# Optimization experiments

Hardware: AMD Instinct MI355X
Metric: run time of the kernel (lower is better)

Reference implementation:

```python
import jax, jax.numpy as jnp
import numpy as np

H = 8          # n_heads
D_HEAD = 64    # head_dim; scores scaled by sqrt(D_HEAD)


def setup_inputs() -> dict:
    key = jax.random.key(0)
    ks = jax.random.split(key, 9)
    B, S, Dm = 8, 1024, 512
    return {
        "input_Q": jax.random.normal(ks[0], (B, S, Dm), jnp.float32),
        "input_K": jax.random.normal(ks[1], (B, S, Dm), jnp.float32),
        "input_V": jax.random.normal(ks[2], (B, S, Dm), jnp.float32),
        "attn_mask": jax.random.randint(ks[3], (B, S, S), 0, 2).astype(bool),
        "edge_encoding": jax.random.normal(ks[4], (B, S, S), jnp.float32),
        "W_Q": jax.random.normal(ks[5], (Dm, Dm), jnp.float32) / np.sqrt(Dm),
        "W_K": jax.random.normal(ks[6], (Dm, Dm), jnp.float32) / np.sqrt(Dm),
        "W_V": jax.random.normal(ks[7], (Dm, Dm), jnp.float32) / np.sqrt(Dm),
        "W_fc": jax.random.normal(ks[8], (Dm, Dm), jnp.float32) / np.sqrt(Dm),
    }


def reference(input_Q, input_K, input_V, attn_mask, edge_encoding, W_Q, W_K, W_V, W_fc):
    B, S, Dm = input_Q.shape
    # project and split heads: [B, H, S, d_head]
    def heads(x, W):
        return (x @ W).reshape(B, S, H, D_HEAD).transpose(0, 2, 1, 3)
    Q = heads(input_Q, W_Q)
    K = heads(input_K, W_K)
    V = heads(input_V, W_V)
    scores = jnp.einsum("bhqd,bhkd->bhqk", Q, K) / np.sqrt(D_HEAD)
    scores = scores + edge_encoding[:, None, :, :]
    scores = jnp.where(attn_mask[:, None, :, :], jnp.float32(-1e9), scores)
    attn = jax.nn.softmax(scores, axis=-1)
    context = jnp.einsum("bhqk,bhkd->bhqd", attn, V)
    context = context.transpose(0, 2, 1, 3).reshape(B, S, Dm)
    output = context @ W_fc
    scores_avg = scores.sum(axis=1) / H  # [B, S, S]
    return output, scores_avg
```

## Files before the change

kernel.cpp:

```cpp
#include <hip/hip_runtime.h>
#include <math.h>

#define B_ 8
#define S_ 1024
#define DM 512
#define H_ 8
#define DH 64

typedef _Float16 h4 __attribute__((ext_vector_type(4)));
typedef _Float16 h8 __attribute__((ext_vector_type(8)));
typedef float f4 __attribute__((ext_vector_type(4)));

#define MFMA16(a, b, c) __builtin_amdgcn_mfma_f32_16x16x32_f16(a, b, c, 0, 0, 0)

__global__ __launch_bounds__(256) void cast_x(
    const float* __restrict__ x0, const float* __restrict__ x1,
    const float* __restrict__ x2, _Float16* __restrict__ y0,
    _Float16* __restrict__ y1, _Float16* __restrict__ y2) {
  const float* x = (blockIdx.y == 0) ? x0 : (blockIdx.y == 1) ? x1 : x2;
  _Float16* y = (blockIdx.y == 0) ? y0 : (blockIdx.y == 1) ? y1 : y2;
  size_t i = (size_t)blockIdx.x * 1024 + (size_t)threadIdx.x * 4;
  float4 v = *(const float4*)(x + i);
  h4 hv = {(_Float16)v.x, (_Float16)v.y, (_Float16)v.z, (_Float16)v.w};
  *(h4*)(y + i) = hv;
}

__global__ __launch_bounds__(256) void cast_w(
    const float* __restrict__ w0, const float* __restrict__ w1,
    const float* __restrict__ w2, const float* __restrict__ w3,
    _Float16* __restrict__ t0, _Float16* __restrict__ t1,
    _Float16* __restrict__ t2, _Float16* __restrict__ t3) {
  const float* W;
  _Float16* T;
  switch (blockIdx.z) {
    case 0: W = w0; T = t0; break;
    case 1: W = w1; T = t1; break;
    case 2: W = w2; T = t2; break;
    default: W = w3; T = t3; break;
  }
  __shared__ _Float16 ts[64][72];
  const int t = threadIdx.x;
  const int r = t >> 2, c0 = (t & 3) * 16;
  const int n0 = blockIdx.x * 64, k0 = blockIdx.y * 64;
#pragma unroll
  for (int i = 0; i < 4; i++) {
    float4 v = *(const float4*)&W[(size_t)(k0 + r) * 512 + n0 + c0 + i * 4];
    h4 hv = {(_Float16)v.x, (_Float16)v.y, (_Float16)v.z, (_Float16)v.w};
    *(h4*)&ts[r][c0 + i * 4] = hv;
  }
  __syncthreads();
  alignas(16) _Float16 outv[16];
#pragma unroll
  for (int i = 0; i < 16; i++) outv[i] = ts[c0 + i][r];
  *(uint4*)&T[(size_t)(n0 + r) * 512 + k0 + c0] = *(uint4*)&outv[0];
  *(uint4*)&T[(size_t)(n0 + r) * 512 + k0 + c0 + 8] = *(uint4*)&outv[8];
}

__global__ __launch_bounds__(256) void gemm_qkv(
    const _Float16* __restrict__ Xq, const _Float16* __restrict__ Xk,
    const _Float16* __restrict__ Xv, const _Float16* __restrict__ Wt,
    _Float16* __restrict__ Qh, _Float16* __restrict__ Kh,
    _Float16* __restrict__ Vth) {
  const int z = blockIdx.z;
  const int id = blockIdx.x + 4 * blockIdx.y;
  const int c = id & 7, r = id >> 3;
  const int by = c + 8 * (r & 7);
  const int bx = r >> 3;
  const _Float16* A = (z == 0) ? Xq : (z == 1) ? Xk : Xv;
  const _Float16* Bt = Wt + (size_t)z * 512 * 512;
  __shared__ _Float16 Sh[128 * 144];
  const int t = threadIdx.x, lane = t & 63, w = t >> 6;
  const int quad = lane >> 4, l16 = lane & 15;
  const int row0 = by * 128, col0 = bx * 128;
  const int wm = (w & 1) * 64, wn = (w >> 1) * 64;
  f4 acc[4][4] = {};
  const _Float16* Ab = A + (size_t)(row0 + wm + l16) * DM + quad * 8;
  const _Float16* Bb = Bt + (size_t)(col0 + wn + l16) * DM + quad * 8;
  for (int k0 = 0; k0 < DM; k0 += 64) {
    h8 af[4][2], bf[4][2];
#pragma unroll
    for (int m = 0; m < 4; m++) {
      const _Float16* ap = Ab + (size_t)m * 16 * DM + k0;
      const _Float16* bp = Bb + (size_t)m * 16 * DM + k0;
      af[m][0] = *(const h8*)ap;
      af[m][1] = *(const h8*)(ap + 32);
      bf[m][0] = *(const h8*)bp;
      bf[m][1] = *(const h8*)(bp + 32);
    }
#pragma unroll
    for (int m = 0; m < 4; m++)
#pragma unroll
      for (int n = 0; n < 4; n++) {
        acc[m][n] = MFMA16(af[m][0], bf[n][0], acc[m][n]);
        acc[m][n] = MFMA16(af[m][1], bf[n][1], acc[m][n]);
      }
  }
  if (z < 2) {
    _Float16* C = (z == 0) ? Qh : Kh;
#pragma unroll
    for (int m = 0; m < 4; m++)
#pragma unroll
      for (int n = 0; n < 4; n++)
#pragma unroll
        for (int reg = 0; reg < 4; reg++)
          Sh[(wm + m * 16 + quad * 4 + reg) * 144 + wn + n * 16 + l16] =
              (_Float16)acc[m][n][reg];
    __syncthreads();
    const int rr = t >> 4;
    const int cs = (t & 15) * 8;
#pragma unroll
    for (int i = 0; i < 8; i++) {
      int row = rr + 16 * i;
      *(uint4*)&C[(size_t)(row0 + row) * DM + col0 + cs] =
          *(uint4*)&Sh[row * 144 + cs];
    }
  } else {
#pragma unroll
    for (int m = 0; m < 4; m++)
#pragma unroll
      for (int n = 0; n < 4; n++) {
        h4 vv = {(_Float16)acc[m][n][0], (_Float16)acc[m][n][1],
                 (_Float16)acc[m][n][2], (_Float16)acc[m][n][3]};
        *(h4*)&Sh[(wn + n * 16 + l16) * 144 + wm + m * 16 + quad * 4] = vv;
      }
    __syncthreads();
    const int rr = t >> 4;
    const int cs = (t & 15) * 8;
    const int b = row0 >> 10, s0 = row0 & 1023;
#pragma unroll
    for (int i = 0; i < 8; i++) {
      int cg = col0 + rr + 16 * i;
      int h = cg >> 6, d = cg & 63;
      *(uint4*)&Vth[((size_t)(b * 8 + h) * 64 + d) * S_ + s0 + cs] =
          *(uint4*)&Sh[(rr + 16 * i) * 144 + cs];
    }
  }
}

__global__ __launch_bounds__(256) void gemm_fc(
    const _Float16* __restrict__ A, const _Float16* __restrict__ Bt,
    float* __restrict__ C) {
  const int id = blockIdx.x + 4 * blockIdx.y;
  const int c = id & 7, r = id >> 3;
  const int by = c + 8 * (r & 15);
  const int bx = r >> 4;
  const int t = threadIdx.x, lane = t & 63, w = t >> 6;
  const int quad = lane >> 4, l16 = lane & 15;
  const int row0 = by * 64, col0 = bx * 128;
  const int wm = (w & 1) * 32, wn = (w >> 1) * 64;
  f4 acc[2][4] = {};
  const _Float16* Ab = A + (size_t)(row0 + wm + l16) * DM + quad * 8;
  const _Float16* Bb = Bt + (size_t)(col0 + wn + l16) * DM + quad * 8;
  for (int k0 = 0; k0 < DM; k0 += 64) {
    h8 af[2][2], bf[4][2];
#pragma unroll
    for (int m = 0; m < 2; m++) {
      const _Float16* ap = Ab + (size_t)m * 16 * DM + k0;
      af[m][0] = *(const h8*)ap;
      af[m][1] = *(const h8*)(ap + 32);
    }
#pragma unroll
    for (int n = 0; n < 4; n++) {
      const _Float16* bp = Bb + (size_t)n * 16 * DM + k0;
      bf[n][0] = *(const h8*)bp;
      bf[n][1] = *(const h8*)(bp + 32);
    }
#pragma unroll
    for (int m = 0; m < 2; m++)
#pragma unroll
      for (int n = 0; n < 4; n++) {
        acc[m][n] = MFMA16(af[m][0], bf[n][0], acc[m][n]);
        acc[m][n] = MFMA16(af[m][1], bf[n][1], acc[m][n]);
      }
  }
#pragma unroll
  for (int m = 0; m < 2; m++)
#pragma unroll
    for (int n = 0; n < 4; n++)
#pragma unroll
      for (int reg = 0; reg < 4; reg++) {
        size_t row = row0 + wm + m * 16 + quad * 4 + reg;
        size_t col = col0 + wn + n * 16 + l16;
        C[row * DM + col] = acc[m][n][reg];
      }
}

__global__ __launch_bounds__(256) void scores_mfma(
    const _Float16* __restrict__ Qh, const _Float16* __restrict__ Kh,
    const int* __restrict__ mask, const float* __restrict__ edge,
    float* __restrict__ out1, _Float16* __restrict__ Ehs) {
  const int b = blockIdx.z;
  const int id = blockIdx.x + 8 * blockIdx.y;
  const int iy = id & 7, jx = id >> 3;
  const int i0 = iy * 128, j0 = jx * 128;
  const _Float16* A = Qh + (size_t)b * S_ * DM;
  const _Float16* Bt = Kh + (size_t)b * S_ * DM;
  const int t = threadIdx.x, lane = t & 63, w = t >> 6;
  const int quad = lane >> 4, l16 = lane & 15;
  const int wm = (w & 1) * 64, wn = (w >> 1) * 64;
  f4 acc[4][4] = {};
  const _Float16* Ab = A + (size_t)(i0 + wm + l16) * DM + quad * 8;
  const _Float16* Bb = Bt + (size_t)(j0 + wn + l16) * DM + quad * 8;
  for (int k0 = 0; k0 < DM; k0 += 64) {
    h8 af[4][2], bf[4][2];
#pragma unroll
    for (int m = 0; m < 4; m++) {
      const _Float16* ap = Ab + (size_t)m * 16 * DM + k0;
      const _Float16* bp = Bb + (size_t)m * 16 * DM + k0;
      af[m][0] = *(const h8*)ap;
      af[m][1] = *(const h8*)(ap + 32);
      bf[m][0] = *(const h8*)bp;
      bf[m][1] = *(const h8*)(bp + 32);
    }
#pragma unroll
    for (int m = 0; m < 4; m++)
#pragma unroll
      for (int n = 0; n < 4; n++) {
        acc[m][n] = MFMA16(af[m][0], bf[n][0], acc[m][n]);
        acc[m][n] = MFMA16(af[m][1], bf[n][1], acc[m][n]);
      }
  }
  const int jt_base = j0 >> 6;
#pragma unroll
  for (int m = 0; m < 4; m++)
#pragma unroll
    for (int reg = 0; reg < 4; reg++) {
      size_t gi = i0 + wm + m * 16 + quad * 4 + reg;
      size_t rowb = ((size_t)b * S_ + gi) * S_;
      const int jt = jt_base + (wn >> 6);
      size_t ehrow = (((size_t)b * 16 + jt) * 1024 + gi) * 64 + l16 * 4;
      h4 ev;
#pragma unroll
      for (int n = 0; n < 4; n++) {
        size_t idx = rowb + j0 + wn + n * 16 + l16;
        int mk = mask[idx];
        float e = edge[idx];
        out1[idx] = mk ? -1e9f : (acc[m][n][reg] * (1.0f / 64.0f) + e);
        ev[n] = mk ? (_Float16)(-65504.0f) : (_Float16)e;
      }
      *(h4*)&Ehs[ehrow] = ev;
    }
}

__global__ __launch_bounds__(256) void flash_mfma(
    const _Float16* __restrict__ Qh, const _Float16* __restrict__ Kh,
    const _Float16* __restrict__ Vth, const _Float16* __restrict__ Ehs,
    _Float16* __restrict__ ctxh) {
  __shared__ _Float16 Ps[128][72], Ks[64][72], Vt[64][72];
  const int t = threadIdx.x, lane = t & 63, w = t >> 6;
  const int quad = lane >> 4, l16 = lane & 15;
  const int g = blockIdx.x + 8 * blockIdx.y;
  const int c = g & 7, r = g >> 3;
  const int bh = c + 8 * (r & 7);
  const int qb = r >> 3;
  const int b = bh >> 3, h = bh & 7;
  const int q0 = qb * 128;
  const size_t bS = (size_t)b * S_;
  const int sr = t >> 3, sc = (t & 7) * 8;
  const int qw = w * 32;

#pragma unroll
  for (int i = 0; i < 4; i++)
    *(uint4*)&Ps[sr + 32 * i][sc] =
        *(const uint4*)&Qh[(bS + q0 + sr + 32 * i) * DM + h * DH + sc];
  __syncthreads();
  h8 aq[2][2];
#pragma unroll
  for (int m = 0; m < 2; m++)
#pragma unroll
    for (int k = 0; k < 2; k++)
      aq[m][k] = *(h8*)&Ps[qw + m * 16 + l16][k * 32 + quad * 8];

  uint4 kv[4];
  kv[0] = *(const uint4*)&Kh[(bS + sr) * DM + h * DH + sc];
  kv[1] = *(const uint4*)&Kh[(bS + sr + 32) * DM + h * DH + sc];
  kv[2] = *(const uint4*)&Vth[((size_t)bh * 64 + sr) * S_ + sc];
  kv[3] = *(const uint4*)&Vth[((size_t)bh * 64 + sr + 32) * S_ + sc];
  h4 evh[2][4];
#pragma unroll
  for (int m = 0; m < 2; m++)
#pragma unroll
    for (int reg = 0; reg < 4; reg++)
      evh[m][reg] = *(const h4*)&Ehs[(((size_t)b * 16 + 0) * 1024 + q0 + qw +
                                      m * 16 + quad * 4 + reg) *
                                         64 +
                                     l16 * 4];

  f4 acco[2][4] = {};
  float m_run[2][4], l_run[2][4];
#pragma unroll
  for (int m = 0; m < 2; m++)
#pragma unroll
    for (int rr = 0; rr < 4; rr++) {
      m_run[m][rr] = -INFINITY;
      l_run[m][rr] = 0.f;
    }

  for (int kb = 0; kb < S_; kb += 64) {
    __syncthreads();
    *(uint4*)&Ks[sr][sc] = kv[0];
    *(uint4*)&Ks[sr + 32][sc] = kv[1];
    *(uint4*)&Vt[sr][sc] = kv[2];
    *(uint4*)&Vt[sr + 32][sc] = kv[3];
    __syncthreads();
    const int kn = kb + 64;
    h4 evn[2][4];
    if (kn < S_) {
      kv[0] = *(const uint4*)&Kh[(bS + kn + sr) * DM + h * DH + sc];
      kv[1] = *(const uint4*)&Kh[(bS + kn + sr + 32) * DM + h * DH + sc];
      kv[2] = *(const uint4*)&Vth[((size_t)bh * 64 + sr) * S_ + kn + sc];
      kv[3] = *(const uint4*)&Vth[((size_t)bh * 64 + sr + 32) * S_ + kn + sc];
      const size_t ehb = ((size_t)b * 16 + (kn >> 6)) * 1024;
#pragma unroll
      for (int m = 0; m < 2; m++)
#pragma unroll
        for (int reg = 0; reg < 4; reg++)
          evn[m][reg] =
              *(const h4*)&Ehs[(ehb + q0 + qw + m * 16 + quad * 4 + reg) * 64 +
                               l16 * 4];
    }
    f4 accs[2][4] = {};
#pragma unroll
    for (int n = 0; n < 4; n++) {
      h8 b0 = *(h8*)&Ks[n * 16 + l16][quad * 8];
      h8 b1 = *(h8*)&Ks[n * 16 + l16][32 + quad * 8];
#pragma unroll
      for (int m = 0; m < 2; m++) {
        accs[m][n] = MFMA16(aq[m][0], b0, accs[m][n]);
        accs[m][n] = MFMA16(aq[m][1], b1, accs[m][n]);
      }
    }
    float sv[2][4][4];
#pragma unroll
    for (int m = 0; m < 2; m++)
#pragma unroll
      for (int n = 0; n < 4; n++)
#pragma unroll
        for (int reg = 0; reg < 4; reg++)
          sv[m][n][reg] = accs[m][n][reg] * 0.125f + (float)evh[m][reg][n];
#pragma unroll
    for (int m = 0; m < 2; m++)
#pragma unroll
      for (int reg = 0; reg < 4; reg++) {
        float mx = fmaxf(fmaxf(sv[m][0][reg], sv[m][1][reg]),
                         fmaxf(sv[m][2][reg], sv[m][3][reg]));
#pragma unroll
        for (int off = 1; off < 16; off <<= 1)
          mx = fmaxf(mx, __shfl_xor(mx, off, 16));
        float mnew = fmaxf(m_run[m][reg], mx);
        float alpha = __expf(m_run[m][reg] - mnew);
        m_run[m][reg] = mnew;
        float psum = 0.f;
#pragma unroll
        for (int n = 0; n < 4; n++) {
          float p = __expf(sv[m][n][reg] - mnew);
          sv[m][n][reg] = p;
          psum += p;
        }
#pragma unroll
        for (int off = 1; off < 16; off <<= 1)
          psum += __shfl_xor(psum, off, 16);
        l_run[m][reg] = l_run[m][reg] * alpha + psum;
#pragma unroll
        for (int d = 0; d < 4; d++) acco[m][d][reg] *= alpha;
      }
#pragma unroll
    for (int m = 0; m < 2; m++)
#pragma unroll
      for (int n = 0; n < 4; n++)
#pragma unroll
        for (int reg = 0; reg < 4; reg++)
          Ps[qw + m * 16 + quad * 4 + reg][n * 16 + l16] =
              (_Float16)sv[m][n][reg];
    h8 ap[2][2];
#pragma unroll
    for (int m = 0; m < 2; m++)
#pragma unroll
      for (int k = 0; k < 2; k++)
        ap[m][k] = *(h8*)&Ps[qw + m * 16 + l16][k * 32 + quad * 8];
#pragma unroll
    for (int d = 0; d < 4; d++) {
      h8 bv0 = *(h8*)&Vt[d * 16 + l16][quad * 8];
      h8 bv1 = *(h8*)&Vt[d * 16 + l16][32 + quad * 8];
#pragma unroll
      for (int m = 0; m < 2; m++) {
        acco[m][d] = MFMA16(ap[m][0], bv0, acco[m][d]);
        acco[m][d] = MFMA16(ap[m][1], bv1, acco[m][d]);
      }
    }
    if (kn < S_) {
#pragma unroll
      for (int m = 0; m < 2; m++)
#pragma unroll
        for (int reg = 0; reg < 4; reg++) evh[m][reg] = evn[m][reg];
    }
  }
#pragma unroll
  for (int m = 0; m < 2; m++)
#pragma unroll
    for (int d = 0; d < 4; d++)
#pragma unroll
      for (int reg = 0; reg < 4; reg++)
        Ps[qw + m * 16 + quad * 4 + reg][d * 16 + l16] =
            (_Float16)(acco[m][d][reg] / l_run[m][reg]);
  __syncthreads();
  const int orr = t >> 3, ocs = (t & 7) * 8;
#pragma unroll
  for (int i = 0; i < 4; i++) {
    int row = orr + 32 * i;
    *(uint4*)&ctxh[(bS + q0 + row) * DM + h * DH + ocs] =
        *(uint4*)&Ps[row][ocs];
  }
}

extern "C" void kernel_launch(void* const* d_in, const int* in_sizes, int n_in,
                              void* d_out, int out_size, void* d_ws,
                              size_t ws_size, hipStream_t stream) {
  const float* Xq = (const float*)d_in[0];
  const float* Xk = (const float*)d_in[1];
  const float* Xv = (const float*)d_in[2];
  const int* mask = (const int*)d_in[3];
  const float* edge = (const float*)d_in[4];
  const float* Wq = (const float*)d_in[5];
  const float* Wk = (const float*)d_in[6];
  const float* Wv = (const float*)d_in[7];
  const float* Wfc = (const float*)d_in[8];

  float* out0 = (float*)d_out;
  float* out1 = out0 + (size_t)B_ * S_ * DM;

  const size_t NE = (size_t)B_ * S_ * DM;
  char* ws = (char*)d_ws;
  _Float16* Qh = (_Float16*)ws;
  _Float16* Kh = Qh + NE;
  _Float16* Vth = Kh + NE;
  _Float16* Xhq = Vth + NE;
  _Float16* Xhk = Xhq + NE;
  _Float16* Xhv = Xhk + NE;
  _Float16* Wt = Xhv + NE;
  _Float16* Wtf = Wt + 3 * 512 * 512;
  _Float16* Ehs = Wt + 4 * 512 * 512;
  _Float16* ctxh = Xhq;

  dim3 blk(256);
  cast_x<<<dim3(4096, 3), blk, 0, stream>>>(Xq, Xk, Xv, Xhq, Xhk, Xhv);
  cast_w<<<dim3(8, 8, 4), blk, 0, stream>>>(Wq, Wk, Wv, Wfc, Wt,
                                            Wt + 512 * 512, Wt + 2 * 512 * 512,
                                            Wtf);
  gemm_qkv<<<dim3(4, 64, 3), blk, 0, stream>>>(Xhq, Xhk, Xhv, Wt, Qh, Kh, Vth);
  scores_mfma<<<dim3(8, 8, 8), blk, 0, stream>>>(Qh, Kh, mask, edge, out1,
                                                 Ehs);
  flash_mfma<<<dim3(8, 64), blk, 0, stream>>>(Qh, Kh, Vth, Ehs, ctxh);
  gemm_fc<<<dim3(4, 128), blk, 0, stream>>>(ctxh, Wtf, out0);
}
```

Baseline: 356.0 us.

## Shrink flash query tile, use lazy max rescaling and MFMA row sums

The flash attention kernel now processes 64 query rows per block (16 per wave) and launches twice as many blocks. It loads Q directly into registers instead of staging through shared memory. It rescales the running accumulators only when the new row max exceeds the old one by more than a threshold (checked wave-wide). The row-sum shuffle reduction is replaced by an MFMA against a ones vector. This cuts shuffles, exps and register pressure and adds parallelism, at the cost of reloading K/V tiles twice as often per query and letting fp16 probabilities reach values up to e^8.

New measurement: 374.6 us. 5.2% more time.

```diff
diff --git a/kernel.cpp b/kernel.cpp
--- a/kernel.cpp
+++ b/kernel.cpp
@@ -246,7 +246,7 @@
     const _Float16* __restrict__ Qh, const _Float16* __restrict__ Kh,
     const _Float16* __restrict__ Vth, const _Float16* __restrict__ Ehs,
     _Float16* __restrict__ ctxh) {
-  __shared__ _Float16 Ps[128][72], Ks[64][72], Vt[64][72];
+  __shared__ _Float16 Ps[64][72], Ks[64][72], Vt[64][72];
   const int t = threadIdx.x, lane = t & 63, w = t >> 6;
   const int quad = lane >> 4, l16 = lane & 15;
   const int g = blockIdx.x + 8 * blockIdx.y;
@@ -254,47 +254,39 @@
   const int bh = c + 8 * (r & 7);
   const int qb = r >> 3;
   const int b = bh >> 3, h = bh & 7;
-  const int q0 = qb * 128;
+  const int q0 = qb * 64;
   const size_t bS = (size_t)b * S_;
   const int sr = t >> 3, sc = (t & 7) * 8;
-  const int qw = w * 32;
-
-#pragma unroll
-  for (int i = 0; i < 4; i++)
-    *(uint4*)&Ps[sr + 32 * i][sc] =
-        *(const uint4*)&Qh[(bS + q0 + sr + 32 * i) * DM + h * DH + sc];
-  __syncthreads();
-  h8 aq[2][2];
-#pragma unroll
-  for (int m = 0; m < 2; m++)
-#pragma unroll
-    for (int k = 0; k < 2; k++)
-      aq[m][k] = *(h8*)&Ps[qw + m * 16 + l16][k * 32 + quad * 8];
+  const int qw = w * 16;
+
+  h8 aq[2];
+#pragma unroll
+  for (int k = 0; k < 2; k++)
+    aq[k] = *(const h8*)&Qh[(bS + q0 + qw + l16) * DM + h * DH + k * 32 +
+                            quad * 8];
 
   uint4 kv[4];
   kv[0] = *(const uint4*)&Kh[(bS + sr) * DM + h * DH + sc];
   kv[1] = *(const uint4*)&Kh[(bS + sr + 32) * DM + h * DH + sc];
   kv[2] = *(const uint4*)&Vth[((size_t)bh * 64 + sr) * S_ + sc];
   kv[3] = *(const uint4*)&Vth[((size_t)bh * 64 + sr + 32) * S_ + sc];
-  h4 evh[2][4];
-#pragma unroll
-  for (int m = 0; m < 2; m++)
-#pragma unroll
-    for (int reg = 0; reg < 4; reg++)
-      evh[m][reg] = *(const h4*)&Ehs[(((size_t)b * 16 + 0) * 1024 + q0 + qw +
-                                      m * 16 + quad * 4 + reg) *
-                                         64 +
-                                     l16 * 4];
-
-  f4 acco[2][4] = {};
-  float m_run[2][4], l_run[2][4];
-#pragma unroll
-  for (int m = 0; m < 2; m++)
-#pragma unroll
-    for (int rr = 0; rr < 4; rr++) {
-      m_run[m][rr] = -INFINITY;
-      l_run[m][rr] = 0.f;
-    }
+  h4 evh[4];
+#pragma unroll
+  for (int reg = 0; reg < 4; reg++)
+    evh[reg] = *(const h4*)&Ehs[((size_t)(b * 16) * 1024 + q0 + qw + quad * 4 +
+                                 reg) *
+                                    64 +
+                                l16 * 4];
+
+  f4 acco[4] = {};
+  f4 accl = {};
+  float m_run[4];
+#pragma unroll
+  for (int rr = 0; rr < 4; rr++) m_run[rr] = -INFINITY;
+
+  h8 vone;
+#pragma unroll
+  for (int i = 0; i < 8; i++) vone[i] = (_Float16)1.0f;
 
   for (int kb = 0; kb < S_; kb += 64) {
     __syncthreads();
@@ -304,7 +296,7 @@
     *(uint4*)&Vt[sr + 32][sc] = kv[3];
     __syncthreads();
     const int kn = kb + 64;
-    h4 evn[2][4];
+    h4 evn[4];
     if (kn < S_) {
       kv[0] = *(const uint4*)&Kh[(bS + kn + sr) * DM + h * DH + sc];
       kv[1] = *(const uint4*)&Kh[(bS + kn + sr + 32) * DM + h * DH + sc];
@@ -312,101 +304,81 @@
       kv[3] = *(const uint4*)&Vth[((size_t)bh * 64 + sr + 32) * S_ + kn + sc];
       const size_t ehb = ((size_t)b * 16 + (kn >> 6)) * 1024;
 #pragma unroll
-      for (int m = 0; m < 2; m++)
-#pragma unroll
-        for (int reg = 0; reg < 4; reg++)
-          evn[m][reg] =
-              *(const h4*)&Ehs[(ehb + q0 + qw + m * 16 + quad * 4 + reg) * 64 +
-                               l16 * 4];
-    }
-    f4 accs[2][4] = {};
+      for (int reg = 0; reg < 4; reg++)
+        evn[reg] = *(const h4*)&Ehs[(ehb + q0 + qw + quad * 4 + reg) * 64 +
+                                    l16 * 4];
+    }
+    f4 accs[4] = {};
 #pragma unroll
     for (int n = 0; n < 4; n++) {
       h8 b0 = *(h8*)&Ks[n * 16 + l16][quad * 8];
       h8 b1 = *(h8*)&Ks[n * 16 + l16][32 + quad * 8];
-#pragma unroll
-      for (int m = 0; m < 2; m++) {
-        accs[m][n] = MFMA16(aq[m][0], b0, accs[m][n]);
-        accs[m][n] = MFMA16(aq[m][1], b1, accs[m][n]);
-      }
-    }
-    float sv[2][4][4];
-#pragma unroll
-    for (int m = 0; m < 2; m++)
-#pragma unroll
-      for (int n = 0; n < 4; n++)
-#pragma unroll
-        for (int reg = 0; reg < 4; reg++)
-          sv[m][n][reg] = accs[m][n][reg] * 0.125f + (float)evh[m][reg][n];
-#pragma unroll
-    for (int m = 0; m < 2; m++)
+      accs[n] = MFMA16(aq[0], b0, accs[n]);
+      accs[n] = MFMA16(aq[1], b1, accs[n]);
+    }
+    float sv[4][4];
+#pragma unroll
+    for (int n = 0; n < 4; n++)
+#pragma unroll
+      for (int reg = 0; reg < 4; reg++)
+        sv[n][reg] = accs[n][reg] * 0.125f + (float)evh[reg][n];
+    float mxr[4];
+#pragma unroll
+    for (int reg = 0; reg < 4; reg++) {
+      float mx = fmaxf(fmaxf(sv[0][reg], sv[1][reg]),
+                       fmaxf(sv[2][reg], sv[3][reg]));
+#pragma unroll
+      for (int off = 1; off < 16; off <<= 1)
+        mx = fmaxf(mx, __shfl_xor(mx, off, 16));
+      mxr[reg] = mx;
+    }
+    int need = 0;
+#pragma unroll
+    for (int reg = 0; reg < 4; reg++)
+      need |= (mxr[reg] > m_run[reg] + 8.0f) ? 1 : 0;
+    if (__any(need)) {
 #pragma unroll
       for (int reg = 0; reg < 4; reg++) {
-        float mx = fmaxf(fmaxf(sv[m][0][reg], sv[m][1][reg]),
-                         fmaxf(sv[m][2][reg], sv[m][3][reg]));
-#pragma unroll
-        for (int off = 1; off < 16; off <<= 1)
-          mx = fmaxf(mx, __shfl_xor(mx, off, 16));
-        float mnew = fmaxf(m_run[m][reg], mx);
-        float alpha = __expf(m_run[m][reg] - mnew);
-        m_run[m][reg] = mnew;
-        float psum = 0.f;
-#pragma unroll
-        for (int n = 0; n < 4; n++) {
-          float p = __expf(sv[m][n][reg] - mnew);
-          sv[m][n][reg] = p;
-          psum += p;
-        }
-#pragma unroll
-        for (int off = 1; off < 16; off <<= 1)
-          psum += __shfl_xor(psum, off, 16);
-        l_run[m][reg] = l_run[m][reg] * alpha + psum;
-#pragma unroll
-        for (int d = 0; d < 4; d++) acco[m][d][reg] *= alpha;
-      }
-#pragma unroll
-    for (int m = 0; m < 2; m++)
-#pragma unroll
-      for (int n = 0; n < 4; n++)
-#pragma unroll
-        for (int reg = 0; reg < 4; reg++)
-          Ps[qw + m * 16 + quad * 4 + reg][n * 16 + l16] =
-              (_Float16)sv[m][n][reg];
-    h8 ap[2][2];
-#pragma unroll
-    for (int m = 0; m < 2; m++)
-#pragma unroll
-      for (int k = 0; k < 2; k++)
-        ap[m][k] = *(h8*)&Ps[qw + m * 16 + l16][k * 32 + quad * 8];
+        float mnew = fmaxf(m_run[reg], mxr[reg]);
+        float al = __expf(m_run[reg] - mnew);
+        m_run[reg] = mnew;
+        accl[reg] *= al;
+#pragma unroll
+        for (int d = 0; d < 4; d++) acco[d][reg] *= al;
+      }
+    }
+#pragma unroll
+    for (int n = 0; n < 4; n++)
+#pragma unroll
+      for (int reg = 0; reg < 4; reg++)
+        Ps[qw + quad * 4 + reg][n * 16 + l16] =
+            (_Float16)__expf(sv[n][reg] - m_run[reg]);
+    h8 ap0 = *(h8*)&Ps[qw + l16][quad * 8];
+    h8 ap1 = *(h8*)&Ps[qw + l16][32 + quad * 8];
 #pragma unroll
     for (int d = 0; d < 4; d++) {
       h8 bv0 = *(h8*)&Vt[d * 16 + l16][quad * 8];
       h8 bv1 = *(h8*)&Vt[d * 16 + l16][32 + quad * 8];
-#pragma unroll
-      for (int m = 0; m < 2; m++) {
-        acco[m][d] = MFMA16(ap[m][0], bv0, acco[m][d]);
-        acco[m][d] = MFMA16(ap[m][1], bv1, acco[m][d]);
-      }
-    }
+      acco[d] = MFMA16(ap0, bv0, acco[d]);
+      acco[d] = MFMA16(ap1, bv1, acco[d]);
+    }
+    accl = MFMA16(ap0, vone, accl);
+    accl = MFMA16(ap1, vone, accl);
     if (kn < S_) {
 #pragma unroll
-      for (int m = 0; m < 2; m++)
-#pragma unroll
-        for (int reg = 0; reg < 4; reg++) evh[m][reg] = evn[m][reg];
-    }
-  }
-#pragma unroll
-  for (int m = 0; m < 2; m++)
-#pragma unroll
-    for (int d = 0; d < 4; d++)
-#pragma unroll
-      for (int reg = 0; reg < 4; reg++)
-        Ps[qw + m * 16 + quad * 4 + reg][d * 16 + l16] =
-            (_Float16)(acco[m][d][reg] / l_run[m][reg]);
+      for (int reg = 0; reg < 4; reg++) evh[reg] = evn[reg];
+    }
+  }
+#pragma unroll
+  for (int d = 0; d < 4; d++)
+#pragma unroll
+    for (int reg = 0; reg < 4; reg++)
+      Ps[qw + quad * 4 + reg][d * 16 + l16] =
+          (_Float16)(acco[d][reg] / accl[reg]);
   __syncthreads();
   const int orr = t >> 3, ocs = (t & 7) * 8;
 #pragma unroll
-  for (int i = 0; i < 4; i++) {
+  for (int i = 0; i < 2; i++) {
     int row = orr + 32 * i;
     *(uint4*)&ctxh[(bS + q0 + row) * DM + h * DH + ocs] =
         *(uint4*)&Ps[row][ocs];
@@ -450,6 +422,6 @@
   gemm_qkv<<<dim3(4, 64, 3), blk, 0, stream>>>(Xhq, Xhk, Xhv, Wt, Qh, Kh, Vth);
   scores_mfma<<<dim3(8, 8, 8), blk, 0, stream>>>(Qh, Kh, mask, edge, out1,
                                                  Ehs);
-  flash_mfma<<<dim3(8, 64), blk, 0, stream>>>(Qh, Kh, Vth, Ehs, ctxh);
+  flash_mfma<<<dim3(8, 128), blk, 0, stream>>>(Qh, Kh, Vth, Ehs, ctxh);
   gemm_fc<<<dim3(4, 128), blk, 0, stream>>>(ctxh, Wtf, out0);
 }
```

## Use lazy max rescaling and MFMA row-sum in flash attention loop

Applied to the files above, without the earlier changes.

The online softmax now rescales the running max and accumulators only when some row's block max exceeds the stored max by more than a threshold, using a wave-wide vote to skip the rescale branch otherwise. The row-sum is computed by an extra MFMA of P against a vector of ones instead of shuffle reductions. A launch bound occupancy hint of two blocks is also added. This removes per-tile exp/shuffle work at the cost of extra MFMAs and a risk of fp16 overflow in P when values up to e^8 are stored.

After: 355.6 us. Within noise of the previous version (-0.1%).

```diff
diff --git a/kernel.cpp b/kernel.cpp
--- a/kernel.cpp
+++ b/kernel.cpp
@@ -242,7 +242,7 @@
     }
 }
 
-__global__ __launch_bounds__(256) void flash_mfma(
+__global__ __launch_bounds__(256, 2) void flash_mfma(
     const _Float16* __restrict__ Qh, const _Float16* __restrict__ Kh,
     const _Float16* __restrict__ Vth, const _Float16* __restrict__ Ehs,
     _Float16* __restrict__ ctxh) {
@@ -287,14 +287,16 @@
                                      l16 * 4];
 
   f4 acco[2][4] = {};
-  float m_run[2][4], l_run[2][4];
+  f4 accl[2] = {};
+  float m_run[2][4];
 #pragma unroll
   for (int m = 0; m < 2; m++)
 #pragma unroll
-    for (int rr = 0; rr < 4; rr++) {
-      m_run[m][rr] = -INFINITY;
-      l_run[m][rr] = 0.f;
-    }
+    for (int rr = 0; rr < 4; rr++) m_run[m][rr] = -INFINITY;
+
+  h8 vone;
+#pragma unroll
+  for (int i = 0; i < 8; i++) vone[i] = (_Float16)1.0f;
 
   for (int kb = 0; kb < S_; kb += 64) {
     __syncthreads();
@@ -338,6 +340,7 @@
 #pragma unroll
         for (int reg = 0; reg < 4; reg++)
           sv[m][n][reg] = accs[m][n][reg] * 0.125f + (float)evh[m][reg][n];
+    float mxr[2][4];
 #pragma unroll
     for (int m = 0; m < 2; m++)
 #pragma unroll
@@ -347,23 +350,27 @@
 #pragma unroll
         for (int off = 1; off < 16; off <<= 1)
           mx = fmaxf(mx, __shfl_xor(mx, off, 16));
-        float mnew = fmaxf(m_run[m][reg], mx);
-        float alpha = __expf(m_run[m][reg] - mnew);
-        m_run[m][reg] = mnew;
-        float psum = 0.f;
-#pragma unroll
-        for (int n = 0; n < 4; n++) {
-          float p = __expf(sv[m][n][reg] - mnew);
-          sv[m][n][reg] = p;
-          psum += p;
+        mxr[m][reg] = mx;
+      }
+    int need = 0;
+#pragma unroll
+    for (int m = 0; m < 2; m++)
+#pragma unroll
+      for (int reg = 0; reg < 4; reg++)
+        need |= (mxr[m][reg] > m_run[m][reg] + 8.0f) ? 1 : 0;
+    if (__any(need)) {
+#pragma unroll
+      for (int m = 0; m < 2; m++)
+#pragma unroll
+        for (int reg = 0; reg < 4; reg++) {
+          float mnew = fmaxf(m_run[m][reg], mxr[m][reg]);
+          float al = __expf(m_run[m][reg] - mnew);
+          m_run[m][reg] = mnew;
+          accl[m][reg] *= al;
+#pragma unroll
+          for (int d = 0; d < 4; d++) acco[m][d][reg] *= al;
         }
-#pragma unroll
-        for (int off = 1; off < 16; off <<= 1)
-          psum += __shfl_xor(psum, off, 16);
-        l_run[m][reg] = l_run[m][reg] * alpha + psum;
-#pragma unroll
-        for (int d = 0; d < 4; d++) acco[m][d][reg] *= alpha;
-      }
+    }
 #pragma unroll
     for (int m = 0; m < 2; m++)
 #pragma unroll
@@ -371,7 +378,7 @@
 #pragma unroll
         for (int reg = 0; reg < 4; reg++)
           Ps[qw + m * 16 + quad * 4 + reg][n * 16 + l16] =
-              (_Float16)sv[m][n][reg];
+              (_Float16)__expf(sv[m][n][reg] - m_run[m][reg]);
     h8 ap[2][2];
 #pragma unroll
     for (int m = 0; m < 2; m++)
@@ -388,6 +395,11 @@
         acco[m][d] = MFMA16(ap[m][1], bv1, acco[m][d]);
       }
     }
+#pragma unroll
+    for (int m = 0; m < 2; m++) {
+      accl[m] = MFMA16(ap[m][0], vone, accl[m]);
+      accl[m] = MFMA16(ap[m][1], vone, accl[m]);
+    }
     if (kn < S_) {
 #pragma unroll
       for (int m = 0; m < 2; m++)
@@ -402,7 +414,7 @@
 #pragma unroll
       for (int reg = 0; reg < 4; reg++)
         Ps[qw + m * 16 + quad * 4 + reg][d * 16 + l16] =
-            (_Float16)(acco[m][d][reg] / l_run[m][reg]);
+            (_Float16)(acco[m][d][reg] / accl[m][reg]);
   __syncthreads();
   const int orr = t >> 3, ocs = (t & 7) * 8;
 #pragma unroll
```
